# Optimization experiments

Hardware: AMD Instinct MI355X
Metric: run time of the kernel (lower is better)

Reference implementation:

```python
import jax, jax.numpy as jnp
import numpy as np

N, IN_F, H, D = 3072, 512, 8, 64


def setup_inputs() -> dict:
    key = jax.random.key(0)
    k1, k2, k3, k4, k5 = jax.random.split(key, 5)
    x = jax.random.normal(k1, (N, IN_F), dtype=jnp.float32)
    adj = jax.random.randint(k2, (N, N), 0, 2, dtype=jnp.int32)
    # xavier-uniform-like scales
    s_W = (6.0 / (IN_F + H * D)) ** 0.5
    s_a = (6.0 / (H + D)) ** 0.5
    W = jax.random.uniform(k3, (H * D, IN_F), dtype=jnp.float32, minval=-s_W, maxval=s_W)
    a_src = jax.random.uniform(k4, (H, D), dtype=jnp.float32, minval=-s_a, maxval=s_a)
    a_dst = jax.random.uniform(k5, (H, D), dtype=jnp.float32, minval=-s_a, maxval=s_a)
    return {"x": x, "adj": adj, "W": W, "a_src": a_src, "a_dst": a_dst}


def reference(x, adj, W, a_src, a_dst):
    n = x.shape[0]
    Hh, d = a_src.shape
    h = (x @ W.T).reshape(n, Hh, d)                      # [n, H, d]
    e_src = jnp.einsum('nhd,hd->nh', h, a_src)           # [n, H]
    e_dst = jnp.einsum('nhd,hd->nh', h, a_dst)           # [n, H]
    e = e_src[:, None, :] + e_dst[None, :, :]            # [n, n, H], e[i,j]=src_i+dst_j
    e = jax.nn.leaky_relu(e, negative_slope=0.2)
    mask = (adj + jnp.eye(n, dtype=adj.dtype)) > 0       # [n, n]
    e = jnp.where(mask[:, :, None], e, -jnp.inf)
    alpha = jax.nn.softmax(e, axis=1)                    # softmax over j (neighbors)
    # out[i,h,d] = sum_j alpha[i,j,h] * h[j,h,d]  (dropout=0 / eval mode)
    out = jnp.einsum('ijh,jhd->ihd', alpha, h)
    return out.reshape(n, Hh * d)                        # concat=True
```

## Files before the change

### kernel.cpp

```cpp
#include <hip/hip_runtime.h>
#include <hip/hip_bf16.h>

typedef __bf16 bf16x8 __attribute__((ext_vector_type(8)));
typedef _Float16 half8 __attribute__((ext_vector_type(8)));
typedef _Float16 half2v __attribute__((ext_vector_type(2)));
typedef short s16x2 __attribute__((ext_vector_type(2)));
typedef float f32x4 __attribute__((ext_vector_type(4)));
typedef float f32x16 __attribute__((ext_vector_type(16)));

#define NROW 3072
#define NF 512
#define NH 8
#define ND 64
#define GEMM_BLOCKS 384
#define BP_BLOCKS 1152

__device__ __forceinline__ unsigned gat_enc_key(float f) {
    unsigned u = __float_as_uint(f);
    return (f < 0.f) ? ~u : (u | 0x80000000u);
}
__device__ __forceinline__ float gat_dec_key(unsigned k) {
    unsigned u = (k & 0x80000000u) ? (k ^ 0x80000000u) : ~k;
    return __uint_as_float(u);
}

__device__ __forceinline__ bf16x8 gat_ld_cvt8(const float* p) {
    float4 f0 = *reinterpret_cast<const float4*>(p);
    float4 f1 = *reinterpret_cast<const float4*>(p + 4);
    bf16x8 o = { (__bf16)f0.x, (__bf16)f0.y, (__bf16)f0.z, (__bf16)f0.w,
                 (__bf16)f1.x, (__bf16)f1.y, (__bf16)f1.z, (__bf16)f1.w };
    return o;
}

__global__ __launch_bounds__(256) void gat_gemm_bp(const float* __restrict__ x,
                                                   const float* __restrict__ W,
                                                   _Float16* __restrict__ hT,
                                                   const int* __restrict__ adj,
                                                   unsigned* __restrict__ bits,
                                                   const float* __restrict__ a_src,
                                                   const float* __restrict__ a_dst,
                                                   float* __restrict__ e_srcT,
                                                   float* __restrict__ e_dstT,
                                                   unsigned* __restrict__ maxkey) {
    __shared__ __align__(16) _Float16 smem[10240];
    __shared__ float ered[2][2][2][32];

    if (blockIdx.x >= GEMM_BLOCKS) {
        int g = (blockIdx.x - GEMM_BLOCKS) * 256 + threadIdx.x;
        int row = g / 96;
        int seg = g - row * 96;
        const int* p = adj + row * NROW + seg * 32;
        unsigned w = 0;
#pragma unroll
        for (int q = 0; q < 8; ++q) {
            int4 v = *reinterpret_cast<const int4*>(p + q * 4);
            unsigned b0 = (v.x > 0) ? 1u : 0u;
            unsigned b1 = (v.y > 0) ? 2u : 0u;
            unsigned b2 = (v.z > 0) ? 4u : 0u;
            unsigned b3 = (v.w > 0) ? 8u : 0u;
            w |= (b0 | b1 | b2 | b3) << (q * 4);
        }
        int d = row - seg * 32;
        if ((unsigned)d < 32u) w |= 1u << d;
        bits[g] = w;
        return;
    }

    int b = blockIdx.x;
    int i0 = (b >> 3) * 64;
    int o0 = (b & 7) * 64;
    int head = b & 7;
    int tid = threadIdx.x;
    int wave = tid >> 6;
    int lane = tid & 63;
    int half = lane >> 5;
    int l31 = lane & 31;
    int wr = wave >> 1;
    int wc = wave & 1;

    __bf16* sA = reinterpret_cast<__bf16*>(smem);
    __bf16* sB = reinterpret_cast<__bf16*>(smem) + 5120;

    int r = tid >> 2;
    int pp = tid & 3;
    const float* gA = x + (i0 + r) * NF + pp * 8;
    const float* gB = W + (o0 + r) * NF + pp * 8;
    int dslot = r * 40 + pp * 8;

    *reinterpret_cast<bf16x8*>(sA + dslot) = gat_ld_cvt8(gA);
    *reinterpret_cast<bf16x8*>(sB + dslot) = gat_ld_cvt8(gB);
    __syncthreads();

    f32x16 acc = {};
    int arow = (wr * 32 + l31) * 40;
    int brow = (wc * 32 + l31) * 40;

    for (int c = 0; c < 16; ++c) {
        bf16x8 na, nb;
        bool more = (c < 15);
        if (more) {
            na = gat_ld_cvt8(gA + (c + 1) * 32);
            nb = gat_ld_cvt8(gB + (c + 1) * 32);
        }
        const __bf16* pa = sA + (c & 1) * 2560;
        const __bf16* pb = sB + (c & 1) * 2560;
#pragma unroll
        for (int ks = 0; ks < 2; ++ks) {
            int q = (((ks << 1) | half)) << 3;
            bf16x8 a = *reinterpret_cast<const bf16x8*>(pa + arow + q);
            bf16x8 bb = *reinterpret_cast<const bf16x8*>(pb + brow + q);
            acc = __builtin_amdgcn_mfma_f32_32x32x16_bf16(a, bb, acc, 0, 0, 0);
        }
        if (more) {
            *reinterpret_cast<bf16x8*>(sA + ((c + 1) & 1) * 2560 + dslot) = na;
            *reinterpret_cast<bf16x8*>(sB + ((c + 1) & 1) * 2560 + dslot) = nb;
        }
        __syncthreads();
    }

    _Float16* tt = smem + wave * 1280;
#pragma unroll
    for (int reg = 0; reg < 16; ++reg) {
        int rowl = (reg & 3) + 8 * (reg >> 2) + 4 * half;
        tt[rowl * 40 + l31] = (_Float16)acc[reg];
    }
    int orow = lane >> 1;
    int li = (lane & 1) * 16;
    half8 h0, h1;
#pragma unroll
    for (int t = 0; t < 8; ++t) h0[t] = tt[(li + t) * 40 + orow];
#pragma unroll
    for (int t = 0; t < 8; ++t) h1[t] = tt[(li + 8 + t) * 40 + orow];
    _Float16* op = hT + (long)(o0 + wc * 32 + orow) * NROW + i0 + wr * 32 + li;
    *reinterpret_cast<half8*>(op) = h0;
    *reinterpret_cast<half8*>(op + 8) = h1;

    half8 hv0 = *reinterpret_cast<const half8*>(tt + l31 * 40 + half * 16);
    half8 hv1 = *reinterpret_cast<const half8*>(tt + l31 * 40 + half * 16 + 8);
    const float* ap = a_src + head * ND + wc * 32 + half * 16;
    const float* dp = a_dst + head * ND + wc * 32 + half * 16;
    float4 as0 = *reinterpret_cast<const float4*>(ap);
    float4 as1 = *reinterpret_cast<const float4*>(ap + 4);
    float4 as2 = *reinterpret_cast<const float4*>(ap + 8);
    float4 as3 = *reinterpret_cast<const float4*>(ap + 12);
    float4 ad0 = *reinterpret_cast<const float4*>(dp);
    float4 ad1 = *reinterpret_cast<const float4*>(dp + 4);
    float4 ad2 = *reinterpret_cast<const float4*>(dp + 8);
    float4 ad3 = *reinterpret_cast<const float4*>(dp + 12);
    float ps = 0.f, pd = 0.f;
    ps += (float)hv0[0]*as0.x + (float)hv0[1]*as0.y + (float)hv0[2]*as0.z + (float)hv0[3]*as0.w;
    ps += (float)hv0[4]*as1.x + (float)hv0[5]*as1.y + (float)hv0[6]*as1.z + (float)hv0[7]*as1.w;
    ps += (float)hv1[0]*as2.x + (float)hv1[1]*as2.y + (float)hv1[2]*as2.z + (float)hv1[3]*as2.w;
    ps += (float)hv1[4]*as3.x + (float)hv1[5]*as3.y + (float)hv1[6]*as3.z + (float)hv1[7]*as3.w;
    pd += (float)hv0[0]*ad0.x + (float)hv0[1]*ad0.y + (float)hv0[2]*ad0.z + (float)hv0[3]*ad0.w;
    pd += (float)hv0[4]*ad1.x + (float)hv0[5]*ad1.y + (float)hv0[6]*ad1.z + (float)hv0[7]*ad1.w;
    pd += (float)hv1[0]*ad2.x + (float)hv1[1]*ad2.y + (float)hv1[2]*ad2.z + (float)hv1[3]*ad2.w;
    pd += (float)hv1[4]*ad3.x + (float)hv1[5]*ad3.y + (float)hv1[6]*ad3.z + (float)hv1[7]*ad3.w;
    ps += __shfl_xor(ps, 32, 64);
    pd += __shfl_xor(pd, 32, 64);
    if (half == 0) { ered[0][wr][wc][l31] = ps; ered[1][wr][wc][l31] = pd; }
    __syncthreads();
    if (wc == 0) {
        float pst = ered[0][wr][0][l31] + ered[0][wr][1][l31];
        float pdt = ered[1][wr][0][l31] + ered[1][wr][1][l31];
        if (half == 0) {
            e_srcT[head * NROW + i0 + wr * 32 + l31] = pst;
            e_dstT[head * NROW + i0 + wr * 32 + l31] = pdt;
        }
        float mx = pdt;
#pragma unroll
        for (int off = 1; off < 32; off <<= 1) mx = fmaxf(mx, __shfl_xor(mx, off, 64));
        if (lane == 0) atomicMax(&maxkey[head], gat_enc_key(mx));
    }
}

__global__ __launch_bounds__(256) void gat_attn(const unsigned* __restrict__ bits,
                                                const float* __restrict__ e_srcT,
                                                const float* __restrict__ e_dstT,
                                                const unsigned* __restrict__ maxkey,
                                                const _Float16* __restrict__ hT,
                                                _Float16* __restrict__ num,
                                                float* __restrict__ den) {
    constexpr int JCHUNK = NROW / 4;
    constexpr int NC = JCHUNK / 64;
    __shared__ unsigned lds_P[JCHUNK / 2];
    __shared__ unsigned lds_Q[JCHUNK / 2];
    __shared__ __align__(16) _Float16 hbuf[2][4096];
    int b = blockIdx.x;
    int head = b & 7;
    int jc = (b >> 3) & 3;
    int i0 = ((b >> 3) >> 2) * 128;
    int jbase = jc * JCHUNK;
    int tid = threadIdx.x;
    int wave = tid >> 6;
    int lane = tid & 63;
    int half = lane >> 5;
    int l31 = lane & 31;

    float Mg = gat_dec_key(maxkey[head]);
    for (int p = tid; p < JCHUNK / 2; p += 256) {
        float t0 = e_dstT[head * NROW + jbase + 2 * p] - Mg;
        float t1 = e_dstT[head * NROW + jbase + 2 * p + 1] - Mg;
        half2v P = { (_Float16)__expf(t0), (_Float16)__expf(t1) };
        half2v Q = { (_Float16)__expf(0.2f * t0), (_Float16)__expf(0.2f * t1) };
        lds_P[p] = __builtin_bit_cast(unsigned, P);
        lds_Q[p] = __builtin_bit_cast(unsigned, Q);
    }

    int irow = i0 + wave * 32 + l31;
    float u = e_srcT[head * NROW + irow] + Mg;
    float Rf = fminf(__expf(-0.8f * u), 60000.f);
    _Float16 Rh = (_Float16)Rf;
    half2v R2 = { Rh, Rh };
    const half8 ones8 = { (_Float16)1.f, (_Float16)1.f, (_Float16)1.f, (_Float16)1.f,
                          (_Float16)1.f, (_Float16)1.f, (_Float16)1.f, (_Float16)1.f };
    const unsigned* brow = bits + irow * 96 + jc * (JCHUNK / 32);

    int s0 = tid, s1 = tid + 256;
    const _Float16* gp0 = hT + (head * ND + ((s0 >> 6) & 1) * 32 + (s0 & 31)) * NROW
                             + jbase + (s0 >> 7) * 16 + ((s0 >> 5) & 1) * 8;
    const _Float16* gp1 = hT + (head * ND + ((s1 >> 6) & 1) * 32 + (s1 & 31)) * NROW
                             + jbase + (s1 >> 7) * 16 + ((s1 >> 5) & 1) * 8;
    *reinterpret_cast<half8*>(&hbuf[0][tid * 8])         = *reinterpret_cast<const half8*>(gp0);
    *reinterpret_cast<half8*>(&hbuf[0][(tid + 256) * 8]) = *reinterpret_cast<const half8*>(gp1);
    __syncthreads();

    f32x16 acc0 = {};
    f32x16 acc1 = {};
    f32x16 acc2 = {};
    uint2 wm = *reinterpret_cast<const uint2*>(brow);

    for (int k = 0; k < NC; ++k) {
        half8 st0, st1;
        uint2 wmn = wm;
        bool more = (k + 1 < NC);
        if (more) {
            st0 = *reinterpret_cast<const half8*>(gp0 + (k + 1) * 64);
            st1 = *reinterpret_cast<const half8*>(gp1 + (k + 1) * 64);
            wmn = *reinterpret_cast<const uint2*>(brow + (k + 1) * 2);
        }
        const _Float16* hb = &hbuf[k & 1][0];
#pragma unroll
        for (int js = 0; js < 4; ++js) {
            unsigned word = (js < 2) ? wm.x : wm.y;
            unsigned w8 = (word >> ((js & 1) * 16 + half * 8)) & 0xffu;
            unsigned long long S64 = ((unsigned long long)(w8 & 0x55u) << 15)
                                   | ((unsigned long long)(w8 & 0xAAu) << 30);
            uint4 Pv = *reinterpret_cast<const uint4*>(&lds_P[k * 32 + js * 8 + half * 4]);
            uint4 Qv = *reinterpret_cast<const uint4*>(&lds_Q[k * 32 + js * 8 + half * 4]);
            unsigned pr[4] = { Pv.x, Pv.y, Pv.z, Pv.w };
            unsigned qr[4] = { Qv.x, Qv.y, Qv.z, Qv.w };
            unsigned am[4];
#pragma unroll
            for (int t = 0; t < 4; ++t) {
                half2v qq = __builtin_bit_cast(half2v, qr[t]) * R2;
                half2v mx = __builtin_elementwise_max(
                                __builtin_bit_cast(half2v, pr[t]), qq);
                unsigned Wt = (unsigned)(S64 >> (2 * t));
                s16x2 mks = __builtin_bit_cast(s16x2, Wt) >> 15;
                am[t] = __builtin_bit_cast(unsigned, mx)
                      & __builtin_bit_cast(unsigned, mks);
            }
            uint4 m4 = { am[0], am[1], am[2], am[3] };
            half8 af = __builtin_bit_cast(half8, m4);
            half8 v0 = *reinterpret_cast<const half8*>(hb + (js * 128 + lane) * 8);
            half8 v1 = *reinterpret_cast<const half8*>(hb + (js * 128 + 64 + lane) * 8);
            acc0 = __builtin_amdgcn_mfma_f32_32x32x16_f16(af, v0, acc0, 0, 0, 0);
            acc1 = __builtin_amdgcn_mfma_f32_32x32x16_f16(af, v1, acc1, 0, 0, 0);
            acc2 = __builtin_amdgcn_mfma_f32_32x32x16_f16(af, ones8, acc2, 0, 0, 0);
        }
        if (more) {
            *reinterpret_cast<half8*>(&hbuf[(k + 1) & 1][tid * 8])         = st0;
            *reinterpret_cast<half8*>(&hbuf[(k + 1) & 1][(tid + 256) * 8]) = st1;
        }
        wm = wmn;
        __syncthreads();
    }

#pragma unroll
    for (int reg = 0; reg < 16; ++reg) {
        int rowl = (reg & 3) + 8 * (reg >> 2) + 4 * half;
        if (l31 == 0)
            den[(long)(jc * NROW + i0 + wave * 32 + rowl) * NH + head] = acc2[reg];
        long ob = (long)(jc * NROW + i0 + wave * 32 + rowl) * NF + head * ND + l31;
        num[ob]      = (_Float16)acc0[reg];
        num[ob + 32] = (_Float16)acc1[reg];
    }
}

__global__ __launch_bounds__(256) void gat_final(const _Float16* __restrict__ num,
                                                 const float* __restrict__ den,
                                                 float* __restrict__ out) {
    int idx = (blockIdx.x * 256 + threadIdx.x) * 8;
    int i = idx >> 9;
    int c = idx & 511;
    int head = c >> 6;
    half8 n0 = *reinterpret_cast<const half8*>(num + (long)i * NF + c);
    half8 n1 = *reinterpret_cast<const half8*>(num + (long)(NROW + i) * NF + c);
    half8 n2 = *reinterpret_cast<const half8*>(num + (long)(2 * NROW + i) * NF + c);
    half8 n3 = *reinterpret_cast<const half8*>(num + (long)(3 * NROW + i) * NF + c);
    float ds = den[i * NH + head] + den[(NROW + i) * NH + head]
             + den[(2 * NROW + i) * NH + head] + den[(3 * NROW + i) * NH + head];
    float inv = 1.0f / fmaxf(ds, 1e-30f);
    float r0 = ((float)n0[0] + (float)n1[0] + (float)n2[0] + (float)n3[0]) * inv;
    float r1 = ((float)n0[1] + (float)n1[1] + (float)n2[1] + (float)n3[1]) * inv;
    float r2 = ((float)n0[2] + (float)n1[2] + (float)n2[2] + (float)n3[2]) * inv;
    float r3 = ((float)n0[3] + (float)n1[3] + (float)n2[3] + (float)n3[3]) * inv;
    float r4 = ((float)n0[4] + (float)n1[4] + (float)n2[4] + (float)n3[4]) * inv;
    float r5 = ((float)n0[5] + (float)n1[5] + (float)n2[5] + (float)n3[5]) * inv;
    float r6 = ((float)n0[6] + (float)n1[6] + (float)n2[6] + (float)n3[6]) * inv;
    float r7 = ((float)n0[7] + (float)n1[7] + (float)n2[7] + (float)n3[7]) * inv;
    float4 o0 = { r0, r1, r2, r3 };
    float4 o1 = { r4, r5, r6, r7 };
    *reinterpret_cast<float4*>(out + idx)     = o0;
    *reinterpret_cast<float4*>(out + idx + 4) = o1;
}

extern "C" void kernel_launch(void* const* d_in, const int* in_sizes, int n_in,
                              void* d_out, int out_size, void* d_ws, size_t ws_size,
                              hipStream_t stream) {
    const float* x_raw  = (const float*)d_in[0];
    const int*   adj    = (const int*)d_in[1];
    const float* W_raw  = (const float*)d_in[2];
    const float* as_raw = (const float*)d_in[3];
    const float* ad_raw = (const float*)d_in[4];
    float* out = (float*)d_out;

    char* ws = (char*)d_ws;
    _Float16* hT     = (_Float16*)(ws);
    float*    e_srcT = (float*)(ws + 3145728);
    float*    e_dstT = (float*)(ws + 3244032);
    unsigned* maxkey = (unsigned*)(ws + 3342336);
    unsigned* bits   = (unsigned*)(ws + 3342400);
    _Float16* num    = (_Float16*)(ws + 8192064);
    float*    den    = (float*)(ws + 20774976);

    hipMemsetAsync(maxkey, 0, 64, stream);
    gat_gemm_bp<<<GEMM_BLOCKS + BP_BLOCKS, 256, 0, stream>>>(x_raw, W_raw, hT, adj,
                                                             bits, as_raw, ad_raw,
                                                             e_srcT, e_dstT, maxkey);
    gat_attn<<<24 * 4 * 8, 256, 0, stream>>>(bits, e_srcT, e_dstT, maxkey, hT, num, den);
    gat_final<<<NROW * NF / 2048, 256, 0, stream>>>(num, den, out);
}
```

Measured before the change: 135.2 us.

## Load GEMM operands directly from global into registers, dropping LDS staging

The projection GEMM no longer stages bf16-converted x and W tiles through double-buffered shared memory with per-step barriers. Each lane instead reads its own fp32 operand fragments from global memory, with a one-step register prefetch, and converts them to bf16 right before each MFMA. This removes LDS traffic and 16 block syncs and shrinks shared memory. In exchange, each A/B element is reloaded by several waves instead of shared, and accesses are narrower and strided per lane, so the kernel leans more on L1/L2 bandwidth.

Result: slower. 145.9 us (+7.9%).

```diff
diff --git a/kernel.cpp b/kernel.cpp
--- a/kernel.cpp
+++ b/kernel.cpp
@@ -22,14 +22,6 @@
 __device__ __forceinline__ float gat_dec_key(unsigned k) {
     unsigned u = (k & 0x80000000u) ? (k ^ 0x80000000u) : ~k;
     return __uint_as_float(u);
-}
-
-__device__ __forceinline__ bf16x8 gat_ld_cvt8(const float* p) {
-    float4 f0 = *reinterpret_cast<const float4*>(p);
-    float4 f1 = *reinterpret_cast<const float4*>(p + 4);
-    bf16x8 o = { (__bf16)f0.x, (__bf16)f0.y, (__bf16)f0.z, (__bf16)f0.w,
-                 (__bf16)f1.x, (__bf16)f1.y, (__bf16)f1.z, (__bf16)f1.w };
-    return o;
 }
 
 __global__ __launch_bounds__(256) void gat_gemm_bp(const float* __restrict__ x,
@@ -42,7 +34,7 @@
                                                    float* __restrict__ e_srcT,
                                                    float* __restrict__ e_dstT,
                                                    unsigned* __restrict__ maxkey) {
-    __shared__ __align__(16) _Float16 smem[10240];
+    __shared__ __align__(16) _Float16 tts[4 * 1280];
     __shared__ float ered[2][2][2][32];
 
     if (blockIdx.x >= GEMM_BLOCKS) {
@@ -78,47 +70,32 @@
     int wr = wave >> 1;
     int wc = wave & 1;
 
-    __bf16* sA = reinterpret_cast<__bf16*>(smem);
-    __bf16* sB = reinterpret_cast<__bf16*>(smem) + 5120;
-
-    int r = tid >> 2;
-    int pp = tid & 3;
-    const float* gA = x + (i0 + r) * NF + pp * 8;
-    const float* gB = W + (o0 + r) * NF + pp * 8;
-    int dslot = r * 40 + pp * 8;
-
-    *reinterpret_cast<bf16x8*>(sA + dslot) = gat_ld_cvt8(gA);
-    *reinterpret_cast<bf16x8*>(sB + dslot) = gat_ld_cvt8(gB);
-    __syncthreads();
+    const float* xr = x + (long)(i0 + wr * 32 + l31) * NF + half * 8;
+    const float* wp = W + (long)(o0 + wc * 32 + l31) * NF + half * 8;
 
     f32x16 acc = {};
-    int arow = (wr * 32 + l31) * 40;
-    int brow = (wc * 32 + l31) * 40;
-
-    for (int c = 0; c < 16; ++c) {
-        bf16x8 na, nb;
-        bool more = (c < 15);
-        if (more) {
-            na = gat_ld_cvt8(gA + (c + 1) * 32);
-            nb = gat_ld_cvt8(gB + (c + 1) * 32);
-        }
-        const __bf16* pa = sA + (c & 1) * 2560;
-        const __bf16* pb = sB + (c & 1) * 2560;
-#pragma unroll
-        for (int ks = 0; ks < 2; ++ks) {
-            int q = (((ks << 1) | half)) << 3;
-            bf16x8 a = *reinterpret_cast<const bf16x8*>(pa + arow + q);
-            bf16x8 bb = *reinterpret_cast<const bf16x8*>(pb + brow + q);
-            acc = __builtin_amdgcn_mfma_f32_32x32x16_bf16(a, bb, acc, 0, 0, 0);
-        }
-        if (more) {
-            *reinterpret_cast<bf16x8*>(sA + ((c + 1) & 1) * 2560 + dslot) = na;
-            *reinterpret_cast<bf16x8*>(sB + ((c + 1) & 1) * 2560 + dslot) = nb;
-        }
-        __syncthreads();
-    }
-
-    _Float16* tt = smem + wave * 1280;
+    float4 a0 = *reinterpret_cast<const float4*>(xr);
+    float4 a1 = *reinterpret_cast<const float4*>(xr + 4);
+    float4 b0 = *reinterpret_cast<const float4*>(wp);
+    float4 b1 = *reinterpret_cast<const float4*>(wp + 4);
+#pragma unroll
+    for (int c = 0; c < 32; ++c) {
+        float4 na0, na1, nb0, nb1;
+        if (c < 31) {
+            na0 = *reinterpret_cast<const float4*>(xr + (c + 1) * 16);
+            na1 = *reinterpret_cast<const float4*>(xr + (c + 1) * 16 + 4);
+            nb0 = *reinterpret_cast<const float4*>(wp + (c + 1) * 16);
+            nb1 = *reinterpret_cast<const float4*>(wp + (c + 1) * 16 + 4);
+        }
+        bf16x8 af = { (__bf16)a0.x, (__bf16)a0.y, (__bf16)a0.z, (__bf16)a0.w,
+                      (__bf16)a1.x, (__bf16)a1.y, (__bf16)a1.z, (__bf16)a1.w };
+        bf16x8 bf = { (__bf16)b0.x, (__bf16)b0.y, (__bf16)b0.z, (__bf16)b0.w,
+                      (__bf16)b1.x, (__bf16)b1.y, (__bf16)b1.z, (__bf16)b1.w };
+        acc = __builtin_amdgcn_mfma_f32_32x32x16_bf16(af, bf, acc, 0, 0, 0);
+        a0 = na0; a1 = na1; b0 = nb0; b1 = nb1;
+    }
+
+    _Float16* tt = tts + wave * 1280;
 #pragma unroll
     for (int reg = 0; reg < 16; ++reg) {
         int rowl = (reg & 3) + 8 * (reg >> 2) + 4 * half;
```
